# Kernel optimization log

Measured on AMD Instinct MI355X. Metric: run time of the kernel, lower is better.

The kernel has to match this reference:

```python
import jax, jax.numpy as jnp
import numpy as np

# RRFU config (matches init_kwargs)
S = 2          # scale_factor
G = 4          # groups
K = 3          # sample_k
C = 64         # in_channels
B, H, W_IN = 4, 128, 128
SC = S * S     # s_c
KC = K * K     # sample_c (3x3 = 9)


def setup_inputs() -> dict:
    key = jax.random.key(0)
    ks = jax.random.split(key, 9)
    x = jax.random.normal(ks[0], (B, C, H, W_IN), jnp.float32)
    # 1x1 conv weights stored as (out_ch, in_ch); std chosen per module's init
    # (mask convs are zero-init in the original; use small random so math is nontrivial)
    w_off = jax.random.normal(ks[1], (G * SC * 2, C), jnp.float32) * 0.001
    b_off = jnp.zeros((G * SC * 2,), jnp.float32)
    w_offm = jax.random.normal(ks[2], (G * SC * 2, C), jnp.float32) * 0.01
    b_offm = jnp.zeros((G * SC * 2,), jnp.float32)
    w_sk = jax.random.normal(ks[3], (KC, C), jnp.float32) * 0.005
    b_sk = jnp.zeros((KC,), jnp.float32)
    w_km = jax.random.normal(ks[4], (KC, C), jnp.float32) * 0.01
    b_km = jnp.zeros((KC,), jnp.float32)
    return {"x": x, "w_off": w_off, "b_off": b_off, "w_offm": w_offm,
            "b_offm": b_offm, "w_sk": w_sk, "b_sk": b_sk, "w_km": w_km, "b_km": b_km}


def _conv1x1(x, w, b):
    return jnp.einsum('oc,bchw->bohw', w, x) + b[None, :, None, None]


def _bilinear_border(img, iy, ix):
    """img: (Cg,H,W); iy,ix: (Ho,Wo) pixel coords. grid_sample bilinear, padding_mode='border'."""
    Hh, Ww = img.shape[1], img.shape[2]
    ix = jnp.clip(ix, 0.0, Ww - 1.0)
    iy = jnp.clip(iy, 0.0, Hh - 1.0)
    x0 = jnp.floor(ix)
    y0 = jnp.floor(iy)
    wx = ix - x0
    wy = iy - y0
    x0i = x0.astype(jnp.int32)
    y0i = y0.astype(jnp.int32)
    x1i = jnp.minimum(x0i + 1, Ww - 1)
    y1i = jnp.minimum(y0i + 1, Hh - 1)
    v00 = img[:, y0i, x0i]
    v01 = img[:, y0i, x1i]
    v10 = img[:, y1i, x0i]
    v11 = img[:, y1i, x1i]
    return (v00 * (1 - wx) * (1 - wy) + v01 * wx * (1 - wy)
            + v10 * (1 - wx) * wy + v11 * wx * wy)


def reference(x, w_off, b_off, w_offm, b_offm, w_sk, b_sk, w_km, b_km):
    b0, c0, h0, w0 = x.shape
    # learned offsets, gated by sigmoid mask
    off = _conv1x1(x, w_off, b_off) * jax.nn.sigmoid(_conv1x1(x, w_offm, b_offm))
    bg = b0 * G
    # (b, g*S*S*2, h, w) -> (bg, S, S, 2, h, w) -> (bg, h, S, w, S, 2) -> (bg, S*h, S*w, 2)
    off = off.reshape(bg, S, S, 2, h0, w0).transpose(0, 4, 1, 5, 2, 3).reshape(bg, S * h0, S * w0, 2)
    Ho, Wo = S * h0, S * w0
    # coord_base + offset, normalized then un-normalized for align_corners=False grid_sample
    cx = jnp.arange(Wo, dtype=x.dtype) + 0.5
    cy = jnp.arange(Ho, dtype=x.dtype) + 0.5
    ix = (cx[None, None, :] + off[..., 0]) * (w0 / Wo) - 0.5  # (bg, Ho, Wo)
    iy = (cy[None, :, None] + off[..., 1]) * (h0 / Ho) - 0.5
    x_r = x.reshape(bg, c0 // G, h0, w0)
    x_def = jax.vmap(_bilinear_border)(x_r, iy, ix).reshape(b0, c0, Ho, Wo)
    # CARAFE-style dynamic reassembly: softmax kernel over 3x3 neighborhood
    sk = _conv1x1(x_def, w_sk, b_sk) * jax.nn.sigmoid(_conv1x1(x_def, w_km, b_km))
    skn = jax.nn.softmax(sk, axis=1)  # (b, 9, Ho, Wo)
    pad = K // 2
    xp = jnp.pad(x_def, ((0, 0), (0, 0), (pad, pad), (pad, pad)))  # zero pad like F.unfold
    out = jnp.zeros_like(x_def)
    for ky in range(K):  # fixed 3x3 taps; avoids materializing (b,c,9,Ho,Wo)
        for kx in range(K):
            out = out + skn[:, ky * K + kx][:, None] * xp[:, :, ky:ky + Ho, kx:kx + Wo]
    return out
```

## Files before the change

kernel.cpp:

```cpp
#include <hip/hip_runtime.h>
#include <hip/hip_fp16.h>

typedef _Float16 h2 __attribute__((ext_vector_type(2)));

constexpr int Bc  = 4;
constexpr int Cc  = 64;
constexpr int H0  = 128;
constexpr int W0  = 128;
constexpr int HW  = H0 * W0;
constexpr int Gc  = 4;
constexpr int HOc = H0 * 2;
constexpr int WOc = W0 * 2;

constexpr int TW = 16;
constexpr int TH = 8;
constexpr int HX = TW + 2;
constexpr int HY = TH + 2;
constexpr int NHALO = HX * HY;
constexpr int NTASK = Gc * NHALO;

constexpr int SXC = 10;
constexpr int SYC = 6;
constexpr int SN  = SXC * SYC;
constexpr int NPAIR = Cc / 2;
constexpr int NSTG  = NPAIR * SN;

union hu32 { unsigned u; h2 h; };

__device__ __forceinline__ float dot2(h2 a, unsigned bw, float c) {
    hu32 cv; cv.u = bw;
#if __has_builtin(__builtin_amdgcn_fdot2)
    return __builtin_amdgcn_fdot2(a, cv.h, c, false);
#else
    return fmaf((float)a[0], (float)cv.h[0],
                fmaf((float)a[1], (float)cv.h[1], c));
#endif
}

__global__ __launch_bounds__(256) void kT_prep(
    const float* __restrict__ w_off, const float* __restrict__ w_offm,
    const float* __restrict__ w_sk,  const float* __restrict__ w_km,
    __half2* __restrict__ wpk0, __half2* __restrict__ wpk)
{
    const int i = blockIdx.x * 256 + threadIdx.x;
    if (i < 2048) {
        const int c2  = i >> 6;
        const int rem = i & 63;
        const int mat = rem >> 5;
        const int r   = rem & 31;
        const float* src = mat ? w_offm : w_off;
        wpk0[i] = __floats2half2_rn(src[r * Cc + 2 * c2],
                                    src[r * Cc + 2 * c2 + 1]);
    } else if (i < 2048 + 576) {
        const int j   = i - 2048;
        const int mat = j >= 288;
        const int jj  = mat ? j - 288 : j;
        const int k   = jj >> 5;
        const int c2  = jj & 31;
        const float* src = mat ? w_km : w_sk;
        wpk[j] = __floats2half2_rn(src[k * Cc + 2 * c2],
                                   src[k * Cc + 2 * c2 + 1]);
    }
}

__global__ __launch_bounds__(256) void k0_offsets(
    const float* __restrict__ x, const unsigned* __restrict__ wpk0,
    const float* __restrict__ b_off, const float* __restrict__ b_offm,
    unsigned* __restrict__ offbuf, unsigned* __restrict__ xt)
{
    __shared__ unsigned xt_lds[64 * 33];
    __shared__ unsigned ob_lds[64 * 17];

    const int b    = blockIdx.y;
    const int t    = threadIdx.x;
    const int wave = t >> 6, lane = t & 63;
    const int r0   = __builtin_amdgcn_readfirstlane(wave * 8);
    const int px   = blockIdx.x * 64 + lane;

    float a[8], m[8];
#pragma unroll
    for (int q = 0; q < 8; ++q) { a[q] = 0.f; m[q] = 0.f; }

    const float*    xp = x + (size_t)b * Cc * HW + px;
    const unsigned* wp = wpk0 + r0;

#pragma unroll 4
    for (int c2 = 0; c2 < NPAIR; ++c2) {
        const float x0 = xp[(2 * c2)     * HW];
        const float x1 = xp[(2 * c2 + 1) * HW];
        hu32 xh; xh.h = h2{(_Float16)x0, (_Float16)x1};
        if (wave == 0) xt_lds[lane * 33 + c2] = xh.u;
#pragma unroll
        for (int q = 0; q < 8; ++q) {
            a[q] = dot2(xh.h, wp[c2 * 64 + q],      a[q]);
            m[q] = dot2(xh.h, wp[c2 * 64 + 32 + q], m[q]);
        }
    }

#pragma unroll
    for (int j = 0; j < 4; ++j) {
        const int r = r0 + 2 * j;
        const float sx = 1.f / (1.f + __expf(-(m[2 * j]     + b_offm[r])));
        const float sy = 1.f / (1.f + __expf(-(m[2 * j + 1] + b_offm[r + 1])));
        const float vx = (a[2 * j]     + b_off[r])     * sx;
        const float vy = (a[2 * j + 1] + b_off[r + 1]) * sy;
        const __half2 hh = __floats2half2_rn(vx, vy);
        union { __half2 h; unsigned u; } cv; cv.h = hh;
        ob_lds[lane * 17 + (r0 >> 1) + j] = cv.u;
    }
    __syncthreads();

    unsigned* xo = xt + ((size_t)b * HW + blockIdx.x * 64) * NPAIR;
#pragma unroll
    for (int it = 0; it < 8; ++it) {
        const int idx = it * 256 + t;
        xo[idx] = xt_lds[(idx >> 5) * 33 + (idx & 31)];
    }
    unsigned* oo = offbuf + ((size_t)b * HW + blockIdx.x * 64) * 16;
#pragma unroll
    for (int it = 0; it < 4; ++it) {
        const int idx = it * 256 + t;
        oo[idx] = ob_lds[(idx >> 4) * 17 + (idx & 15)];
    }
}

__global__ __launch_bounds__(256) void k1_fused(
    const unsigned* __restrict__ xt, const unsigned* __restrict__ offbuf,
    const unsigned* __restrict__ wsku, const float* __restrict__ b_sk,
    const float* __restrict__ b_km,
    float* __restrict__ out)
{
    __shared__ h2       xd2[NPAIR][NHALO];
    __shared__ unsigned xs_u[NSTG];
    __shared__ unsigned short kmbh[128 * 9];
    __shared__ unsigned sknb[128 * 9];

    const unsigned* wkmu = wsku + 288;

    const int b    = blockIdx.y;
    const int tp   = blockIdx.x;
    const int ox = (tp & 15) * TW;
    const int oyb = (tp >> 4) * (2 * TH);
    const int t  = threadIdx.x;
    const int sxr = (ox >> 1) - 1;
    const int syr0 = (oyb >> 1) - 1;
    const int syr1 = syr0 + (TH >> 1);

    const unsigned* xtb = xt + (size_t)b * HW * NPAIR;
    const unsigned* obu = offbuf + (size_t)b * HW * 16;

    unsigned pre0[8], pre1[8];
#pragma unroll
    for (int k = 0; k < 8; ++k) {
        const int i = t + k * 256;
        if (i < NSTG) {
            const int c2  = i & 31;
            const int pos = i >> 5;
            const int r   = pos / SXC;
            const int j   = pos - r * SXC;
            const int xx  = min(max(sxr + j, 0), W0 - 1);
            const int yy0 = min(max(syr0 + r, 0), H0 - 1);
            const int yy1 = min(max(syr1 + r, 0), H0 - 1);
            pre0[k] = xtb[(yy0 * W0 + xx) * NPAIR + c2];
            pre1[k] = xtb[(yy1 * W0 + xx) * NPAIR + c2];
        }
    }
#pragma unroll
    for (int k = 0; k < 8; ++k) {
        const int i = t + k * 256;
        if (i < NSTG) {
            const int c2 = i & 31, pos = i >> 5;
            xs_u[c2 * SN + pos] = pre0[k];
        }
    }
    __syncthreads();

    for (int yt = 0; yt < 2; ++yt) {
        const int oy  = oyb + yt * TH;
        const int syr = yt ? syr1 : syr0;
        const h2* xstage2 = (const h2*)xs_u;

        for (int task = t; task < NTASK; task += 256) {
            const int g   = task / NHALO;
            const int pix = task - g * NHALO;
            const int hy  = pix / HX;
            const int hx  = pix - hy * HX;
            const int gy  = oy - 1 + hy;
            const int gx  = ox - 1 + hx;
            if (gy < 0 || gy >= HOc || gx < 0 || gx >= WOc) {
#pragma unroll
                for (int p = 0; p < 8; ++p) xd2[g * 8 + p][pix] = (h2)0;
                continue;
            }
            const int sy = gy & 1, sx = gx & 1;
            const int h  = gy >> 1, w  = gx >> 1;
            hu32 o2u; o2u.u = obu[(size_t)(h * W0 + w) * 16 + g * 4 + sy * 2 + sx];
            const float offx = (float)o2u.h[0];
            const float offy = (float)o2u.h[1];

            float ix = ((float)gx + 0.5f + offx) * 0.5f - 0.5f;
            float iy = ((float)gy + 0.5f + offy) * 0.5f - 0.5f;
            ix = fminf(fmaxf(ix, 0.f), (float)(W0 - 1));
            iy = fminf(fmaxf(iy, 0.f), (float)(H0 - 1));
            const float x0f = floorf(ix), y0f = floorf(iy);
            const float wx = ix - x0f,   wy = iy - y0f;
            const int x0 = (int)x0f, y0 = (int)y0f;
            const int x1 = min(x0 + 1, W0 - 1), y1 = min(y0 + 1, H0 - 1);
            const float w00 = (1.f - wx) * (1.f - wy);
            const float w01 = wx * (1.f - wy);
            const float w10 = (1.f - wx) * wy;
            const float w11 = wx * wy;

            const int j0 = x0 - sxr, j1 = x1 - sxr;
            const int i0 = y0 - syr, i1 = y1 - syr;
            const bool inl = (j0 >= 0) & (j1 < SXC) & (i0 >= 0) & (i1 < SYC);

            const _Float16 W00 = (_Float16)w00, W01 = (_Float16)w01;
            const _Float16 W10 = (_Float16)w10, W11 = (_Float16)w11;

            if (inl) {
                const int o00 = i0 * SXC + j0, o01 = i0 * SXC + j1;
                const int o10 = i1 * SXC + j0, o11 = i1 * SXC + j1;
                const h2* s2 = xstage2 + (g * 8) * SN;
#pragma unroll
                for (int p = 0; p < 8; ++p) {
                    const h2* pc = s2 + p * SN;
                    xd2[g * 8 + p][pix] =
                        pc[o00] * W00 + pc[o01] * W01 + pc[o10] * W10 + pc[o11] * W11;
                }
            } else {
                const int o00 = (y0 * W0 + x0) * NPAIR, o01 = (y0 * W0 + x1) * NPAIR;
                const int o10 = (y1 * W0 + x0) * NPAIR, o11 = (y1 * W0 + x1) * NPAIR;
#pragma unroll
                for (int p = 0; p < 8; ++p) {
                    const int c2 = g * 8 + p;
                    hu32 v00, v01, v10, v11;
                    v00.u = xtb[o00 + c2]; v01.u = xtb[o01 + c2];
                    v10.u = xtb[o10 + c2]; v11.u = xtb[o11 + c2];
                    xd2[c2][pix] =
                        v00.h * W00 + v01.h * W01 + v10.h * W10 + v11.h * W11;
                }
            }
        }
        __syncthreads();

        if (yt == 0) {
#pragma unroll
            for (int k = 0; k < 8; ++k) {
                const int i = t + k * 256;
                if (i < NSTG) {
                    const int c2 = i & 31, pos = i >> 5;
                    xs_u[c2 * SN + pos] = pre1[k];
                }
            }
        }

        {
            const int p   = t & 127;
            const int ctr = ((p >> 4) + 1) * HX + (p & 15) + 1;
            h2 xv[NPAIR];
#pragma unroll
            for (int c2 = 0; c2 < NPAIR; ++c2) xv[c2] = xd2[c2][ctr];

            float acc[9];
            if (t < 128) {
#pragma unroll
                for (int k = 0; k < 9; ++k) {
                    float a = 0.f;
#pragma unroll
                    for (int c2 = 0; c2 < NPAIR; ++c2)
                        a = dot2(xv[c2], wsku[k * 32 + c2], a);
                    acc[k] = a;
                }
            } else {
#pragma unroll
                for (int k = 0; k < 9; ++k) {
                    float a = 0.f;
#pragma unroll
                    for (int c2 = 0; c2 < NPAIR; ++c2)
                        a = dot2(xv[c2], wkmu[k * 32 + c2], a);
                    kmbh[p * 9 + k] = __half_as_ushort(__float2half(a));
                }
            }
            __syncthreads();

            if (t < 128) {
                float sv[9], mx = -1e30f;
#pragma unroll
                for (int k = 0; k < 9; ++k) {
                    const float z = __half2float(__ushort_as_half(kmbh[p * 9 + k]))
                                    + b_km[k];
                    sv[k] = (acc[k] + b_sk[k]) / (1.f + __expf(-z));
                    mx = fmaxf(mx, sv[k]);
                }
                float sum = 0.f;
#pragma unroll
                for (int k = 0; k < 9; ++k) { sv[k] = __expf(sv[k] - mx); sum += sv[k]; }
                const float inv = 1.f / sum;
#pragma unroll
                for (int k = 0; k < 9; ++k) {
                    const unsigned hu = __half_as_ushort(__float2half(sv[k] * inv));
                    sknb[p * 9 + k] = hu | (hu << 16);
                }
            }
        }
        __syncthreads();

        {
            const int sq    = t & 31;
            const int chunk = t >> 5;
            const int sqx = sq & 7, sqy = sq >> 3;
            const int hx0 = 2 * sqx, hy0 = 2 * sqy;
            const int p00 = (2 * sqy) * TW + 2 * sqx;

            hu32 s00[9], s01[9], s10[9], s11[9];
#pragma unroll
            for (int k = 0; k < 9; ++k) {
                s00[k].u = sknb[p00 * 9 + k];        s01[k].u = sknb[(p00 + 1) * 9 + k];
                s10[k].u = sknb[(p00 + TW) * 9 + k]; s11[k].u = sknb[(p00 + TW + 1) * 9 + k];
            }
            const int orow0 = oy + 2 * sqy, ocol0 = ox + 2 * sqx;

#pragma unroll
            for (int i = 0; i < 4; ++i) {
                const int pr = chunk * 4 + i;
                h2 wd[4][4];
#pragma unroll
                for (int ry = 0; ry < 4; ++ry) {
                    const int base = (hy0 + ry) * HX + hx0;
#pragma unroll
                    for (int rx = 0; rx < 4; ++rx)
                        wd[ry][rx] = xd2[pr][base + rx];
                }
                h2 a00 = (h2)0, a01 = (h2)0, a10 = (h2)0, a11 = (h2)0;
#pragma unroll
                for (int ky = 0; ky < 3; ++ky)
#pragma unroll
                    for (int kx = 0; kx < 3; ++kx) {
                        const int k = ky * 3 + kx;
                        a00 += s00[k].h * wd[ky    ][kx    ];
                        a01 += s01[k].h * wd[ky    ][kx + 1];
                        a10 += s10[k].h * wd[ky + 1][kx    ];
                        a11 += s11[k].h * wd[ky + 1][kx + 1];
                    }
                float* ob0 = out + ((size_t)(b * Cc + 2 * pr)) * (HOc * WOc)
                                 + (size_t)orow0 * WOc + ocol0;
                float* ob1 = ob0 + (size_t)(HOc * WOc);
                *reinterpret_cast<float2*>(ob0)       = make_float2((float)a00[0], (float)a01[0]);
                *reinterpret_cast<float2*>(ob0 + WOc) = make_float2((float)a10[0], (float)a11[0]);
                *reinterpret_cast<float2*>(ob1)       = make_float2((float)a00[1], (float)a01[1]);
                *reinterpret_cast<float2*>(ob1 + WOc) = make_float2((float)a10[1], (float)a11[1]);
            }
        }
        __syncthreads();
    }
}

extern "C" void kernel_launch(void* const* d_in, const int* in_sizes, int n_in,
                              void* d_out, int out_size, void* d_ws, size_t ws_size,
                              hipStream_t stream)
{
    const float* x      = (const float*)d_in[0];
    const float* w_off  = (const float*)d_in[1];
    const float* b_off  = (const float*)d_in[2];
    const float* w_offm = (const float*)d_in[3];
    const float* b_offm = (const float*)d_in[4];
    const float* w_sk   = (const float*)d_in[5];
    const float* b_sk   = (const float*)d_in[6];
    const float* w_km   = (const float*)d_in[7];
    const float* b_km   = (const float*)d_in[8];
    float* outp = (float*)d_out;

    const size_t off_bytes  = (size_t)Bc * HW * 16 * sizeof(unsigned);
    const size_t xt_bytes   = (size_t)Bc * HW * NPAIR * sizeof(unsigned);
    const size_t wpk0_bytes = 2048 * sizeof(__half2);
    const size_t wpk_bytes  = 576 * sizeof(__half2);
    if (ws_size < off_bytes + xt_bytes + wpk0_bytes + wpk_bytes) return;
    unsigned* offbuf = (unsigned*)d_ws;
    unsigned* xtbuf  = (unsigned*)((char*)d_ws + off_bytes);
    __half2*  wpk0   = (__half2*)((char*)d_ws + off_bytes + xt_bytes);
    __half2*  wpk    = (__half2*)((char*)d_ws + off_bytes + xt_bytes + wpk0_bytes);

    dim3 blk(256);
    hipLaunchKernelGGL(kT_prep, dim3(11), blk, 0, stream,
                       w_off, w_offm, w_sk, w_km, wpk0, wpk);

    dim3 g0(HW / 64, Bc);
    hipLaunchKernelGGL(k0_offsets, g0, blk, 0, stream,
                       x, (const unsigned*)wpk0, b_off, b_offm, offbuf, xtbuf);

    dim3 g1(256, Bc);
    hipLaunchKernelGGL(k1_fused, g1, blk, 0, stream,
                       xtbuf, offbuf, (const unsigned*)wpk, b_sk, b_km, outp);
}
```

Before: 55.00 us.

## Pack deformed halo as 8-channel vectors in LDS for 128-bit accesses

Changes the shared-memory layout of the deformed halo tile from per-channel-pair planes to 8-half vectors, with 4 channel pairs per pixel, so the bilinear writer, the kernel-predictor reads and the reassembly stage each use 16-byte LDS accesses. The softmax kernel buffer is padded from 9 to 12 entries per pixel so it can be read with uint4 loads. The reassembly loop is reordered to load each halo row once and update all 4 channel pairs. This cuts the LDS instruction count, but the 16-byte stride may cause bank conflicts and more registers are live at once.

```diff
diff --git a/kernel.cpp b/kernel.cpp
--- a/kernel.cpp
+++ b/kernel.cpp
@@ -2,6 +2,7 @@
 #include <hip/hip_fp16.h>
 
 typedef _Float16 h2 __attribute__((ext_vector_type(2)));
+typedef _Float16 h8 __attribute__((ext_vector_type(8)));
 
 constexpr int Bc  = 4;
 constexpr int Cc  = 64;
@@ -26,6 +27,7 @@
 constexpr int NSTG  = NPAIR * SN;
 
 union hu32 { unsigned u; h2 h; };
+union hq  { h8 a; h2 b[4]; };
 
 __device__ __forceinline__ float dot2(h2 a, unsigned bw, float c) {
     hu32 cv; cv.u = bw;
@@ -130,10 +132,10 @@
     const float* __restrict__ b_km,
     float* __restrict__ out)
 {
-    __shared__ h2       xd2[NPAIR][NHALO];
+    __shared__ __align__(16) h8 xd2q[8 * NHALO];
     __shared__ unsigned xs_u[NSTG];
     __shared__ unsigned short kmbh[128 * 9];
-    __shared__ unsigned sknb[128 * 9];
+    __shared__ __align__(16) unsigned sknb[128 * 12];
 
     const unsigned* wkmu = wsku + 288;
 
@@ -188,8 +190,8 @@
             const int gy  = oy - 1 + hy;
             const int gx  = ox - 1 + hx;
             if (gy < 0 || gy >= HOc || gx < 0 || gx >= WOc) {
-#pragma unroll
-                for (int p = 0; p < 8; ++p) xd2[g * 8 + p][pix] = (h2)0;
+                xd2q[(g * 2)     * NHALO + pix] = (h8)0;
+                xd2q[(g * 2 + 1) * NHALO + pix] = (h8)0;
                 continue;
             }
             const int sy = gy & 1, sx = gx & 1;
@@ -218,6 +220,7 @@
             const _Float16 W00 = (_Float16)w00, W01 = (_Float16)w01;
             const _Float16 W10 = (_Float16)w10, W11 = (_Float16)w11;
 
+            h2 v[8];
             if (inl) {
                 const int o00 = i0 * SXC + j0, o01 = i0 * SXC + j1;
                 const int o10 = i1 * SXC + j0, o11 = i1 * SXC + j1;
@@ -225,8 +228,8 @@
 #pragma unroll
                 for (int p = 0; p < 8; ++p) {
                     const h2* pc = s2 + p * SN;
-                    xd2[g * 8 + p][pix] =
-                        pc[o00] * W00 + pc[o01] * W01 + pc[o10] * W10 + pc[o11] * W11;
+                    v[p] = pc[o00] * W00 + pc[o01] * W01
+                         + pc[o10] * W10 + pc[o11] * W11;
                 }
             } else {
                 const int o00 = (y0 * W0 + x0) * NPAIR, o01 = (y0 * W0 + x1) * NPAIR;
@@ -237,10 +240,14 @@
                     hu32 v00, v01, v10, v11;
                     v00.u = xtb[o00 + c2]; v01.u = xtb[o01 + c2];
                     v10.u = xtb[o10 + c2]; v11.u = xtb[o11 + c2];
-                    xd2[c2][pix] =
-                        v00.h * W00 + v01.h * W01 + v10.h * W10 + v11.h * W11;
-                }
-            }
+                    v[p] = v00.h * W00 + v01.h * W01 + v10.h * W10 + v11.h * W11;
+                }
+            }
+            hq pk0, pk1;
+            pk0.b[0] = v[0]; pk0.b[1] = v[1]; pk0.b[2] = v[2]; pk0.b[3] = v[3];
+            pk1.b[0] = v[4]; pk1.b[1] = v[5]; pk1.b[2] = v[6]; pk1.b[3] = v[7];
+            xd2q[(g * 2)     * NHALO + pix] = pk0.a;
+            xd2q[(g * 2 + 1) * NHALO + pix] = pk1.a;
         }
         __syncthreads();
 
@@ -260,7 +267,11 @@
             const int ctr = ((p >> 4) + 1) * HX + (p & 15) + 1;
             h2 xv[NPAIR];
 #pragma unroll
-            for (int c2 = 0; c2 < NPAIR; ++c2) xv[c2] = xd2[c2][ctr];
+            for (int q = 0; q < 8; ++q) {
+                hq u; u.a = xd2q[q * NHALO + ctr];
+                xv[q * 4 + 0] = u.b[0]; xv[q * 4 + 1] = u.b[1];
+                xv[q * 4 + 2] = u.b[2]; xv[q * 4 + 3] = u.b[3];
+            }
 
             float acc[9];
             if (t < 128) {
@@ -300,56 +311,82 @@
 #pragma unroll
                 for (int k = 0; k < 9; ++k) {
                     const unsigned hu = __half_as_ushort(__float2half(sv[k] * inv));
-                    sknb[p * 9 + k] = hu | (hu << 16);
+                    sknb[p * 12 + k] = hu | (hu << 16);
                 }
             }
         }
         __syncthreads();
 
         {
-            const int sq    = t & 31;
-            const int chunk = t >> 5;
+            const int sq = t & 31;
+            const int q  = t >> 5;
             const int sqx = sq & 7, sqy = sq >> 3;
             const int hx0 = 2 * sqx, hy0 = 2 * sqy;
             const int p00 = (2 * sqy) * TW + 2 * sqx;
 
             hu32 s00[9], s01[9], s10[9], s11[9];
-#pragma unroll
-            for (int k = 0; k < 9; ++k) {
-                s00[k].u = sknb[p00 * 9 + k];        s01[k].u = sknb[(p00 + 1) * 9 + k];
-                s10[k].u = sknb[(p00 + TW) * 9 + k]; s11[k].u = sknb[(p00 + TW + 1) * 9 + k];
+            {
+                const uint4* c0 = (const uint4*)&sknb[p00 * 12];
+                const uint4* c1 = (const uint4*)&sknb[(p00 + 1) * 12];
+                const uint4* c2 = (const uint4*)&sknb[(p00 + TW) * 12];
+                const uint4* c3 = (const uint4*)&sknb[(p00 + TW + 1) * 12];
+                uint4 a0 = c0[0], a1 = c0[1];
+                s00[0].u=a0.x; s00[1].u=a0.y; s00[2].u=a0.z; s00[3].u=a0.w;
+                s00[4].u=a1.x; s00[5].u=a1.y; s00[6].u=a1.z; s00[7].u=a1.w;
+                s00[8].u = sknb[p00 * 12 + 8];
+                uint4 b0 = c1[0], b1 = c1[1];
+                s01[0].u=b0.x; s01[1].u=b0.y; s01[2].u=b0.z; s01[3].u=b0.w;
+                s01[4].u=b1.x; s01[5].u=b1.y; s01[6].u=b1.z; s01[7].u=b1.w;
+                s01[8].u = sknb[(p00 + 1) * 12 + 8];
+                uint4 d0 = c2[0], d1 = c2[1];
+                s10[0].u=d0.x; s10[1].u=d0.y; s10[2].u=d0.z; s10[3].u=d0.w;
+                s10[4].u=d1.x; s10[5].u=d1.y; s10[6].u=d1.z; s10[7].u=d1.w;
+                s10[8].u = sknb[(p00 + TW) * 12 + 8];
+                uint4 e0 = c3[0], e1 = c3[1];
+                s11[0].u=e0.x; s11[1].u=e0.y; s11[2].u=e0.z; s11[3].u=e0.w;
+                s11[4].u=e1.x; s11[5].u=e1.y; s11[6].u=e1.z; s11[7].u=e1.w;
+                s11[8].u = sknb[(p00 + TW + 1) * 12 + 8];
             }
             const int orow0 = oy + 2 * sqy, ocol0 = ox + 2 * sqx;
 
+            h2 A00[4], A01[4], A10[4], A11[4];
 #pragma unroll
             for (int i = 0; i < 4; ++i) {
-                const int pr = chunk * 4 + i;
-                h2 wd[4][4];
-#pragma unroll
-                for (int ry = 0; ry < 4; ++ry) {
-                    const int base = (hy0 + ry) * HX + hx0;
-#pragma unroll
-                    for (int rx = 0; rx < 4; ++rx)
-                        wd[ry][rx] = xd2[pr][base + rx];
-                }
-                h2 a00 = (h2)0, a01 = (h2)0, a10 = (h2)0, a11 = (h2)0;
-#pragma unroll
-                for (int ky = 0; ky < 3; ++ky)
-#pragma unroll
-                    for (int kx = 0; kx < 3; ++kx) {
-                        const int k = ky * 3 + kx;
-                        a00 += s00[k].h * wd[ky    ][kx    ];
-                        a01 += s01[k].h * wd[ky    ][kx + 1];
-                        a10 += s10[k].h * wd[ky + 1][kx    ];
-                        a11 += s11[k].h * wd[ky + 1][kx + 1];
+                A00[i] = (h2)0; A01[i] = (h2)0; A10[i] = (h2)0; A11[i] = (h2)0;
+            }
+
+#pragma unroll
+            for (int ry = 0; ry < 4; ++ry) {
+                const int base = q * NHALO + (hy0 + ry) * HX + hx0;
+                hq w0, w1, w2, w3;
+                w0.a = xd2q[base];     w1.a = xd2q[base + 1];
+                w2.a = xd2q[base + 2]; w3.a = xd2q[base + 3];
+#pragma unroll
+                for (int i = 0; i < 4; ++i) {
+                    const h2 x0 = w0.b[i], x1 = w1.b[i], x2 = w2.b[i], x3 = w3.b[i];
+                    if (ry < 3) {
+                        const int k = ry * 3;
+                        A00[i] += s00[k].h * x0 + s00[k+1].h * x1 + s00[k+2].h * x2;
+                        A01[i] += s01[k].h * x1 + s01[k+1].h * x2 + s01[k+2].h * x3;
                     }
+                    if (ry >= 1) {
+                        const int k = (ry - 1) * 3;
+                        A10[i] += s10[k].h * x0 + s10[k+1].h * x1 + s10[k+2].h * x2;
+                        A11[i] += s11[k].h * x1 + s11[k+1].h * x2 + s11[k+2].h * x3;
+                    }
+                }
+            }
+
+#pragma unroll
+            for (int i = 0; i < 4; ++i) {
+                const int pr = q * 4 + i;
                 float* ob0 = out + ((size_t)(b * Cc + 2 * pr)) * (HOc * WOc)
                                  + (size_t)orow0 * WOc + ocol0;
                 float* ob1 = ob0 + (size_t)(HOc * WOc);
-                *reinterpret_cast<float2*>(ob0)       = make_float2((float)a00[0], (float)a01[0]);
-                *reinterpret_cast<float2*>(ob0 + WOc) = make_float2((float)a10[0], (float)a11[0]);
-                *reinterpret_cast<float2*>(ob1)       = make_float2((float)a00[1], (float)a01[1]);
-                *reinterpret_cast<float2*>(ob1 + WOc) = make_float2((float)a10[1], (float)a11[1]);
+                *reinterpret_cast<float2*>(ob0)       = make_float2((float)A00[i][0], (float)A01[i][0]);
+                *reinterpret_cast<float2*>(ob0 + WOc) = make_float2((float)A10[i][0], (float)A11[i][0]);
+                *reinterpret_cast<float2*>(ob1)       = make_float2((float)A00[i][1], (float)A01[i][1]);
+                *reinterpret_cast<float2*>(ob1 + WOc) = make_float2((float)A10[i][1], (float)A11[i][1]);
             }
         }
         __syncthreads();
```

After: 55.93 us. No clear change (+1.7%).
